# Performance work log

Hardware: AMD Instinct MI355X
Metric: run time of the kernel (lower is better)

## Reference

```python
import jax, jax.numpy as jnp
import numpy as np

TOKENS = 8192      # batch*seq flattened
D_IN = 2048        # in_features (power of 2 for Hadamard)
D_OUT = 8192       # out_features

try:
    FP8 = jnp.float8_e4m3fn
except AttributeError:
    FP8 = None


def fwht(x):
    """Normalized fast Walsh-Hadamard transform over last dim (power of 2)."""
    orig_shape = x.shape
    n = orig_shape[-1]
    x = x.reshape(-1, n)
    h = 1
    while h < n:
        x = x.reshape(-1, n // (2 * h), 2, h)
        a = x[..., 0, :]
        b = x[..., 1, :]
        x = jnp.stack([a + b, a - b], axis=-2).reshape(-1, n)
        h *= 2
    return (x * (1.0 / np.sqrt(n))).reshape(orig_shape)


def setup_inputs() -> dict:
    key = jax.random.key(0)
    kx, kw, kb = jax.random.split(key, 3)
    x = jax.random.normal(kx, (TOKENS, D_IN), dtype=jnp.float32)
    # Weight is stored in fp8 e4m3 (quantized in the Hadamard domain);
    # we materialize its dequantized fp32 values for the reference math.
    w = jax.random.normal(kw, (D_OUT, D_IN), dtype=jnp.float32) * 0.02
    if FP8 is not None:
        w = w.astype(FP8).astype(jnp.float32)  # simulate fp8 storage round-trip
    b = jax.random.normal(kb, (D_OUT,), dtype=jnp.float32) * 0.01
    return {"x": x, "weight": w, "bias": b}


def reference(x, weight, bias):
    # use_hadamard=True: rotate activations into the Hadamard domain
    # (weight was quantized in that domain), then fp8-dequant GEMM + bias.
    x_h = fwht(x)                               # [T, D_IN]
    out = jnp.einsum('td,od->to', x_h, weight)  # [T, D_OUT]
    return out + bias[None, :]
```

## Files before the change

kernel.cpp:

```cpp
#include <hip/hip_runtime.h>
#include <hip/hip_bf16.h>
#include <stdint.h>

#define TOKENS 8192
#define D_IN   2048
#define D_OUT  8192
#define BK     64
#define NT     (D_IN / BK)

typedef __attribute__((ext_vector_type(8))) short short8;
typedef __attribute__((ext_vector_type(4))) float floatx4;

__device__ __forceinline__ void async_copy16(const void* g, void* l) {
    __builtin_amdgcn_global_load_lds((const __attribute__((address_space(1))) void*)g,
                                     (__attribute__((address_space(3))) void*)l,
                                     16, 0, 0);
}

__device__ __forceinline__ void fwht8(float* e) {
#pragma unroll
    for (int s = 1; s < 8; s <<= 1) {
#pragma unroll
        for (int j = 0; j < 8; ++j) {
            if ((j & s) == 0) {
                float a = e[j], b = e[j | s];
                e[j]     = a + b;
                e[j | s] = a - b;
            }
        }
    }
}

__global__ __launch_bounds__(256) void fwht_kernel(const float* __restrict__ x,
                                                   __hip_bfloat16* __restrict__ xh) {
    __shared__ float row[D_IN];
    const int r = blockIdx.x;
    const int t = threadIdx.x;
    const float* xr = x + (size_t)r * D_IN;

    float e[8];
#pragma unroll
    for (int j = 0; j < 8; ++j) e[j] = xr[t + 256 * j];
    fwht8(e);
#pragma unroll
    for (int j = 0; j < 8; ++j) row[t + 256 * j] = e[j];
    __syncthreads();

    float f[8];
#pragma unroll
    for (int j = 0; j < 8; ++j) f[j] = row[8 * t + j];
    fwht8(f);
#pragma unroll
    for (int m = 1; m <= 16; m <<= 1) {
#pragma unroll
        for (int j = 0; j < 8; ++j) {
            float v = __shfl_xor(f[j], m, 64);
            f[j] = (t & m) ? (v - f[j]) : (f[j] + v);
        }
    }

    const float scale = 0.02209708691207961f;
    __hip_bfloat16 ob[8];
#pragma unroll
    for (int j = 0; j < 8; ++j) ob[j] = __float2bfloat16(f[j] * scale);
    __hip_bfloat16* orow = xh + (size_t)r * D_IN + 8 * t;
    *reinterpret_cast<int4*>(orow) = *reinterpret_cast<int4*>(ob);
}

__global__ __launch_bounds__(256) void wconv_kernel(const float* __restrict__ w,
                                                    __hip_bfloat16* __restrict__ wb) {
    const size_t i = ((size_t)blockIdx.x * 256 + threadIdx.x) * 8;
    float4 a = *reinterpret_cast<const float4*>(w + i);
    float4 b = *reinterpret_cast<const float4*>(w + i + 4);
    __hip_bfloat16 ob[8];
    ob[0] = __float2bfloat16(a.x); ob[1] = __float2bfloat16(a.y);
    ob[2] = __float2bfloat16(a.z); ob[3] = __float2bfloat16(a.w);
    ob[4] = __float2bfloat16(b.x); ob[5] = __float2bfloat16(b.y);
    ob[6] = __float2bfloat16(b.z); ob[7] = __float2bfloat16(b.w);
    *reinterpret_cast<int4*>(wb + i) = *reinterpret_cast<int4*>(ob);
}

__global__ __launch_bounds__(512, 2) void gemm_kernel(const __hip_bfloat16* __restrict__ A,
                                                      const __hip_bfloat16* __restrict__ B,
                                                      const float* __restrict__ bias,
                                                      float* __restrict__ C) {
    extern __shared__ float4 smem_f4[];
    __hip_bfloat16* sA = (__hip_bfloat16*)smem_f4;
    __hip_bfloat16* sB = sA + 2 * 16384;

    const int tid    = threadIdx.x;
    const int wave   = tid >> 6;
    const int lane   = tid & 63;
    const int lane16 = lane & 15;
    const int lgrp   = lane >> 4;

    const int bid = blockIdx.x;
    const int xcd = bid & 7;
    const int loc = bid >> 3;
    const int rnd = loc >> 5;
    const int pos = loc & 31;
    const int bm  = xcd * 4 + (pos >> 3);
    const int bn  = rnd * 8 + (pos & 7);

    const int wm = wave >> 2;
    const int wn = wave & 3;

    const int srow = lane >> 3;
    const int scc8 = ((lane & 7) ^ srow) * 8;
    const int r0   = wave * 16 + srow;
    const __hip_bfloat16* gAst = A + (size_t)(bm * 256) * D_IN + scc8;
    const __hip_bfloat16* gBst = B + (size_t)(bn * 256) * D_IN + scc8;

    auto stageA = [&](int kt, int h) {
        const __hip_bfloat16* g = gAst + (size_t)(h * 128 + r0) * D_IN + kt * BK;
        __hip_bfloat16* l = sA + (kt & 1) * 16384 + h * 8192 + wave * 1024;
        async_copy16(g, l);
        async_copy16(g + (size_t)8 * D_IN, l + 512);
    };
    auto stageB = [&](int kt, int h) {
        const __hip_bfloat16* g = gBst + (size_t)(h * 128 + r0) * D_IN + kt * BK;
        __hip_bfloat16* l = sB + (kt & 1) * 16384 + h * 8192 + wave * 1024;
        async_copy16(g, l);
        async_copy16(g + (size_t)8 * D_IN, l + 512);
    };

    const int sw   = lane16 & 7;
    const int cK0  = ((0 + lgrp) ^ sw) * 8;
    const int cK1  = ((4 + lgrp) ^ sw) * 8;
    const int arow = wm * 128 + lane16;
    const int brow = wn * 64  + lane16;

    floatx4 acc[8][4];
#pragma unroll
    for (int m = 0; m < 8; ++m)
#pragma unroll
        for (int n = 0; n < 4; ++n) acc[m][n] = 0;

    stageA(0, 0); stageA(0, 1);
    stageB(0, 0); stageB(0, 1);
    stageA(1, 0); stageA(1, 1);
    asm volatile("s_waitcnt vmcnt(4)" ::: "memory");
    asm volatile("s_barrier" ::: "memory");

    short8 af[8][2];
    short8 bf[4][2];

#pragma unroll 2
    for (int kt = 0; kt < NT; ++kt) {
        const __hip_bfloat16* aB = sA + ((kt & 1) << 14);
        const __hip_bfloat16* bB = sB + ((kt & 1) << 14);

#pragma unroll
        for (int m = 0; m < 4; ++m) {
            const __hip_bfloat16* p = aB + (arow + m * 16) * 64;
            af[m][0] = *reinterpret_cast<const short8*>(p + cK0);
            af[m][1] = *reinterpret_cast<const short8*>(p + cK1);
        }
#pragma unroll
        for (int n = 0; n < 2; ++n) {
            const __hip_bfloat16* p = bB + (brow + n * 16) * 64;
            bf[n][0] = *reinterpret_cast<const short8*>(p + cK0);
            bf[n][1] = *reinterpret_cast<const short8*>(p + cK1);
        }
        if (kt + 1 < NT) stageB(kt + 1, 0);
        asm volatile("s_barrier" ::: "memory");
        __builtin_amdgcn_s_setprio(1);
#pragma unroll
        for (int m = 0; m < 4; ++m)
#pragma unroll
            for (int n = 0; n < 2; ++n) {
                acc[m][n] = __builtin_amdgcn_mfma_f32_16x16x32_bf16(af[m][0], bf[n][0], acc[m][n], 0, 0, 0);
                acc[m][n] = __builtin_amdgcn_mfma_f32_16x16x32_bf16(af[m][1], bf[n][1], acc[m][n], 0, 0, 0);
            }
        __builtin_amdgcn_s_setprio(0);
        asm volatile("s_barrier" ::: "memory");

#pragma unroll
        for (int m = 4; m < 8; ++m) {
            const __hip_bfloat16* p = aB + (arow + m * 16) * 64;
            af[m][0] = *reinterpret_cast<const short8*>(p + cK0);
            af[m][1] = *reinterpret_cast<const short8*>(p + cK1);
        }
        if (kt + 1 < NT) stageB(kt + 1, 1);
        asm volatile("s_barrier" ::: "memory");
        __builtin_amdgcn_s_setprio(1);
#pragma unroll
        for (int m = 4; m < 8; ++m)
#pragma unroll
            for (int n = 0; n < 2; ++n) {
                acc[m][n] = __builtin_amdgcn_mfma_f32_16x16x32_bf16(af[m][0], bf[n][0], acc[m][n], 0, 0, 0);
                acc[m][n] = __builtin_amdgcn_mfma_f32_16x16x32_bf16(af[m][1], bf[n][1], acc[m][n], 0, 0, 0);
            }
        __builtin_amdgcn_s_setprio(0);
        asm volatile("s_barrier" ::: "memory");

#pragma unroll
        for (int n = 2; n < 4; ++n) {
            const __hip_bfloat16* p = bB + (brow + n * 16) * 64;
            bf[n][0] = *reinterpret_cast<const short8*>(p + cK0);
            bf[n][1] = *reinterpret_cast<const short8*>(p + cK1);
        }
        if (kt + 2 < NT) stageA(kt + 2, 0);
        asm volatile("s_barrier" ::: "memory");
        __builtin_amdgcn_s_setprio(1);
#pragma unroll
        for (int m = 0; m < 4; ++m)
#pragma unroll
            for (int n = 2; n < 4; ++n) {
                acc[m][n] = __builtin_amdgcn_mfma_f32_16x16x32_bf16(af[m][0], bf[n][0], acc[m][n], 0, 0, 0);
                acc[m][n] = __builtin_amdgcn_mfma_f32_16x16x32_bf16(af[m][1], bf[n][1], acc[m][n], 0, 0, 0);
            }
        __builtin_amdgcn_s_setprio(0);
        asm volatile("s_barrier" ::: "memory");

        if (kt + 2 < NT) stageA(kt + 2, 1);
        asm volatile("s_barrier" ::: "memory");
        __builtin_amdgcn_s_setprio(1);
#pragma unroll
        for (int m = 4; m < 8; ++m)
#pragma unroll
            for (int n = 2; n < 4; ++n) {
                acc[m][n] = __builtin_amdgcn_mfma_f32_16x16x32_bf16(af[m][0], bf[n][0], acc[m][n], 0, 0, 0);
                acc[m][n] = __builtin_amdgcn_mfma_f32_16x16x32_bf16(af[m][1], bf[n][1], acc[m][n], 0, 0, 0);
            }
        __builtin_amdgcn_s_setprio(0);
        if (kt + 2 < NT) {
            asm volatile("s_waitcnt vmcnt(4)" ::: "memory");
        } else {
            asm volatile("s_waitcnt vmcnt(0)" ::: "memory");
        }
        asm volatile("s_barrier" ::: "memory");
    }

    float bv[4];
#pragma unroll
    for (int n = 0; n < 4; ++n) bv[n] = bias[bn * 256 + wn * 64 + n * 16 + lane16];

#pragma unroll
    for (int m = 0; m < 8; ++m) {
        const int rbase = bm * 256 + wm * 128 + m * 16 + lgrp * 4;
#pragma unroll
        for (int n = 0; n < 4; ++n) {
            const int col = bn * 256 + wn * 64 + n * 16 + lane16;
#pragma unroll
            for (int r = 0; r < 4; ++r) {
                __builtin_nontemporal_store(acc[m][n][r] + bv[n],
                                            &C[(size_t)(rbase + r) * D_OUT + col]);
            }
        }
    }
}

extern "C" void kernel_launch(void* const* d_in, const int* in_sizes, int n_in,
                              void* d_out, int out_size, void* d_ws, size_t ws_size,
                              hipStream_t stream) {
    const float* x    = (const float*)d_in[0];
    const float* w    = (const float*)d_in[1];
    const float* bias = (const float*)d_in[2];
    float* out = (float*)d_out;

    __hip_bfloat16* xh = (__hip_bfloat16*)d_ws;
    __hip_bfloat16* wb = xh + (size_t)TOKENS * D_IN;

    static bool attr_set = false;
    if (!attr_set) {
        (void)hipFuncSetAttribute((const void*)gemm_kernel,
                                  hipFuncAttributeMaxDynamicSharedMemorySize, 131072);
        attr_set = true;
    }

    fwht_kernel<<<TOKENS, 256, 0, stream>>>(x, xh);
    wconv_kernel<<<(D_OUT * D_IN / 8) / 256, 256, 0, stream>>>(w, wb);
    gemm_kernel<<<1024, 512, 131072, stream>>>(xh, wb, bias, out);
}
```

Before: 580.4 us.

## Software-pipeline LDS fragment loads across iterations and reorder MFMA quadrants

Restructures the main GEMM loop so LDS fragment reads for the next k-tile happen during the current tile's MFMA phases. The register fragments are preloaded before the loop, the quadrant order becomes (0-3,0-1),(0-3,2-3),(4-7,2-3),(4-7,0-1), and the vmcnt wait is tightened around the stage-A prefetch. This aims to hide LDS read latency behind MFMA work and cut idle phases between barriers, at the cost of more complex buffer-hazard reasoning. The output store also switches from nontemporal to a plain store.

```diff
diff --git a/kernel.cpp b/kernel.cpp
--- a/kernel.cpp
+++ b/kernel.cpp
@@ -144,24 +144,31 @@
 
     short8 af[8][2];
     short8 bf[4][2];
+#pragma unroll
+    for (int m = 0; m < 4; ++m) {
+        const __hip_bfloat16* p = sA + (arow + m * 16) * 64;
+        af[m][0] = *reinterpret_cast<const short8*>(p + cK0);
+        af[m][1] = *reinterpret_cast<const short8*>(p + cK1);
+    }
+#pragma unroll
+    for (int n = 0; n < 4; ++n) {
+        const __hip_bfloat16* p = sB + (brow + n * 16) * 64;
+        bf[n][0] = *reinterpret_cast<const short8*>(p + cK0);
+        bf[n][1] = *reinterpret_cast<const short8*>(p + cK1);
+    }
 
 #pragma unroll 2
     for (int kt = 0; kt < NT; ++kt) {
-        const __hip_bfloat16* aB = sA + ((kt & 1) << 14);
-        const __hip_bfloat16* bB = sB + ((kt & 1) << 14);
-
-#pragma unroll
-        for (int m = 0; m < 4; ++m) {
-            const __hip_bfloat16* p = aB + (arow + m * 16) * 64;
+        const __hip_bfloat16* curA = sA + ((kt & 1) << 14);
+        const __hip_bfloat16* nxtA = sA + (((kt + 1) & 1) << 14);
+        const __hip_bfloat16* nxtB = sB + (((kt + 1) & 1) << 14);
+
+#pragma unroll
+        for (int m = 4; m < 8; ++m) {
+            const __hip_bfloat16* p = curA + (arow + m * 16) * 64;
             af[m][0] = *reinterpret_cast<const short8*>(p + cK0);
             af[m][1] = *reinterpret_cast<const short8*>(p + cK1);
         }
-#pragma unroll
-        for (int n = 0; n < 2; ++n) {
-            const __hip_bfloat16* p = bB + (brow + n * 16) * 64;
-            bf[n][0] = *reinterpret_cast<const short8*>(p + cK0);
-            bf[n][1] = *reinterpret_cast<const short8*>(p + cK1);
-        }
         if (kt + 1 < NT) stageB(kt + 1, 0);
         asm volatile("s_barrier" ::: "memory");
         __builtin_amdgcn_s_setprio(1);
@@ -175,35 +182,10 @@
         __builtin_amdgcn_s_setprio(0);
         asm volatile("s_barrier" ::: "memory");
 
-#pragma unroll
-        for (int m = 4; m < 8; ++m) {
-            const __hip_bfloat16* p = aB + (arow + m * 16) * 64;
-            af[m][0] = *reinterpret_cast<const short8*>(p + cK0);
-            af[m][1] = *reinterpret_cast<const short8*>(p + cK1);
-        }
         if (kt + 1 < NT) stageB(kt + 1, 1);
         asm volatile("s_barrier" ::: "memory");
         __builtin_amdgcn_s_setprio(1);
 #pragma unroll
-        for (int m = 4; m < 8; ++m)
-#pragma unroll
-            for (int n = 0; n < 2; ++n) {
-                acc[m][n] = __builtin_amdgcn_mfma_f32_16x16x32_bf16(af[m][0], bf[n][0], acc[m][n], 0, 0, 0);
-                acc[m][n] = __builtin_amdgcn_mfma_f32_16x16x32_bf16(af[m][1], bf[n][1], acc[m][n], 0, 0, 0);
-            }
-        __builtin_amdgcn_s_setprio(0);
-        asm volatile("s_barrier" ::: "memory");
-
-#pragma unroll
-        for (int n = 2; n < 4; ++n) {
-            const __hip_bfloat16* p = bB + (brow + n * 16) * 64;
-            bf[n][0] = *reinterpret_cast<const short8*>(p + cK0);
-            bf[n][1] = *reinterpret_cast<const short8*>(p + cK1);
-        }
-        if (kt + 2 < NT) stageA(kt + 2, 0);
-        asm volatile("s_barrier" ::: "memory");
-        __builtin_amdgcn_s_setprio(1);
-#pragma unroll
         for (int m = 0; m < 4; ++m)
 #pragma unroll
             for (int n = 2; n < 4; ++n) {
@@ -213,23 +195,60 @@
         __builtin_amdgcn_s_setprio(0);
         asm volatile("s_barrier" ::: "memory");
 
-        if (kt + 2 < NT) stageA(kt + 2, 1);
-        asm volatile("s_barrier" ::: "memory");
-        __builtin_amdgcn_s_setprio(1);
-#pragma unroll
-        for (int m = 4; m < 8; ++m)
-#pragma unroll
-            for (int n = 2; n < 4; ++n) {
-                acc[m][n] = __builtin_amdgcn_mfma_f32_16x16x32_bf16(af[m][0], bf[n][0], acc[m][n], 0, 0, 0);
-                acc[m][n] = __builtin_amdgcn_mfma_f32_16x16x32_bf16(af[m][1], bf[n][1], acc[m][n], 0, 0, 0);
-            }
-        __builtin_amdgcn_s_setprio(0);
         if (kt + 2 < NT) {
-            asm volatile("s_waitcnt vmcnt(4)" ::: "memory");
+            stageA(kt + 2, 0);
+            asm volatile("s_waitcnt vmcnt(2)" ::: "memory");
         } else {
             asm volatile("s_waitcnt vmcnt(0)" ::: "memory");
         }
         asm volatile("s_barrier" ::: "memory");
+        if (kt + 1 < NT) {
+#pragma unroll
+            for (int m = 0; m < 4; ++m) {
+                const __hip_bfloat16* p = nxtA + (arow + m * 16) * 64;
+                af[m][0] = *reinterpret_cast<const short8*>(p + cK0);
+                af[m][1] = *reinterpret_cast<const short8*>(p + cK1);
+            }
+        }
+        __builtin_amdgcn_s_setprio(1);
+#pragma unroll
+        for (int m = 4; m < 8; ++m)
+#pragma unroll
+            for (int n = 2; n < 4; ++n) {
+                acc[m][n] = __builtin_amdgcn_mfma_f32_16x16x32_bf16(af[m][0], bf[n][0], acc[m][n], 0, 0, 0);
+                acc[m][n] = __builtin_amdgcn_mfma_f32_16x16x32_bf16(af[m][1], bf[n][1], acc[m][n], 0, 0, 0);
+            }
+        __builtin_amdgcn_s_setprio(0);
+        asm volatile("s_barrier" ::: "memory");
+
+        if (kt + 2 < NT) stageA(kt + 2, 1);
+        if (kt + 1 < NT) {
+#pragma unroll
+            for (int n = 2; n < 4; ++n) {
+                const __hip_bfloat16* p = nxtB + (brow + n * 16) * 64;
+                bf[n][0] = *reinterpret_cast<const short8*>(p + cK0);
+                bf[n][1] = *reinterpret_cast<const short8*>(p + cK1);
+            }
+        }
+        asm volatile("s_barrier" ::: "memory");
+        __builtin_amdgcn_s_setprio(1);
+#pragma unroll
+        for (int m = 4; m < 8; ++m)
+#pragma unroll
+            for (int n = 0; n < 2; ++n) {
+                acc[m][n] = __builtin_amdgcn_mfma_f32_16x16x32_bf16(af[m][0], bf[n][0], acc[m][n], 0, 0, 0);
+                acc[m][n] = __builtin_amdgcn_mfma_f32_16x16x32_bf16(af[m][1], bf[n][1], acc[m][n], 0, 0, 0);
+            }
+        __builtin_amdgcn_s_setprio(0);
+        if (kt + 1 < NT) {
+#pragma unroll
+            for (int n = 0; n < 2; ++n) {
+                const __hip_bfloat16* p = nxtB + (brow + n * 16) * 64;
+                bf[n][0] = *reinterpret_cast<const short8*>(p + cK0);
+                bf[n][1] = *reinterpret_cast<const short8*>(p + cK1);
+            }
+        }
+        asm volatile("s_barrier" ::: "memory");
     }
 
     float bv[4];
@@ -244,8 +263,7 @@
             const int col = bn * 256 + wn * 64 + n * 16 + lane16;
 #pragma unroll
             for (int r = 0; r < 4; ++r) {
-                __builtin_nontemporal_store(acc[m][n][r] + bv[n],
-                                            &C[(size_t)(rbase + r) * D_OUT + col]);
+                C[(size_t)(rbase + r) * D_OUT + col] = acc[m][n][r] + bv[n];
             }
         }
     }
```

New measurement: 642.0 us. +10.6%, slower.
